# Optimization experiments

Measured on AMD Instinct MI355X. Metric: run time of the kernel, lower is better.

The kernel has to match this reference:

```python
import jax, jax.numpy as jnp
from jax import lax
import numpy as np

BOHR = 0.52917721067  # Angstrom per Bohr (au.BOHR)
DAMP_MUTUAL = 0.39
DAMP_FIELD = 0.7
N_ITER = 7  # fixed-point iterations for induced dipoles


def setup_inputs() -> dict:
    key = jax.random.key(0)
    N = 100000
    deg = 32
    E = N * deg
    k1, k2, k3, k4, k5, k6, k7 = jax.random.split(key, 7)
    edge_src = jax.random.randint(k1, (E,), 0, N)
    edge_dst = jax.random.randint(k2, (E,), 0, N)
    # realistic interatomic distances in [1, 6] Angstrom (avoid r ~ 0)
    distances = 1.0 + 5.0 * jax.random.uniform(k3, (E,), dtype=jnp.float32)
    u = jax.random.normal(k4, (E, 3), dtype=jnp.float32)
    u = u / jnp.linalg.norm(u, axis=-1, keepdims=True)
    vec = u * distances[:, None]  # consistent |vec| == distances
    polarisability = 0.5 + 1.5 * jax.random.uniform(k5, (N,), dtype=jnp.float32)
    charges = 0.3 * jax.random.normal(k6, (N,), dtype=jnp.float32)
    species = jax.random.randint(k7, (N,), 1, 10)
    return {
        "species": species,
        "edge_src": edge_src,
        "edge_dst": edge_dst,
        "distances": distances,
        "vec": vec,
        "polarisability": polarisability,
        "charges": charges,
    }


def reference(species, edge_src, edge_dst, distances, vec, polarisability, charges):
    N = polarisability.shape[0]
    # convert to atomic units
    rij = distances / BOHR                      # [E]
    vec_ij = vec / BOHR                         # [E,3]
    pol = polarisability.reshape(-1) / BOHR**3  # [N]

    # Thole damping: u_ij^3 = r^3 / sqrt(alpha_i * alpha_j)
    alpha_ij = pol[edge_src] * pol[edge_dst]
    uij3 = rij**3 / jnp.sqrt(alpha_ij)
    exp_m = jnp.exp(-DAMP_MUTUAL * uij3)
    l3_m = 1.0 - exp_m
    l5_m = 1.0 - (1.0 + DAMP_MUTUAL * uij3) * exp_m
    l3_f = 1.0 - jnp.exp(-DAMP_FIELD * uij3)

    inv_r3 = 1.0 / rij**3
    inv_r5 = inv_r3 / rij**2

    # permanent (charge) electric field at src atoms, Thole-damped
    e_edges = (l3_f * charges[edge_dst] * inv_r3)[:, None] * vec_ij  # [E,3]
    E0 = jax.ops.segment_sum(e_edges, edge_src, num_segments=N)      # [N,3]

    alpha = pol[:, None]  # isotropic polarisability [N,1]

    def matvec(mu):
        # Thole-damped dipole-dipole interaction tensor applied to mu: (T mu)_i
        mu_d = mu[edge_dst]                                   # [E,3]
        dot = jnp.sum(vec_ij * mu_d, axis=-1)                 # [E]
        t = (l3_m * inv_r3)[:, None] * mu_d \
            - (3.0 * l5_m * inv_r5 * dot)[:, None] * vec_ij   # [E,3]
        return jax.ops.segment_sum(t, edge_src, num_segments=N)

    # iterative induced dipoles: mu = alpha * (E0 - T mu)
    mu0 = alpha * E0

    def step(mu, _):
        return alpha * (E0 - matvec(mu)), None

    mu, _ = lax.scan(step, mu0, None, length=N_ITER)

    # per-atom polarisation energy: -1/2 mu . E0
    energy = -0.5 * jnp.sum(mu * E0, axis=-1)  # [N]
    return energy
```

## Files before the change

### kernel.cpp

```cpp
#include <hip/hip_runtime.h>
#include <hip/hip_fp16.h>


static constexpr float INV_B  = 1.0f / 0.52917721067f;
static constexpr float INV_B3 = INV_B * INV_B * INV_B;
static constexpr float DM = 0.39f;
static constexpr float DF = 0.7f;
static constexpr int   NITER = 7;
#define SCAN_B 1024
#define STAGE 2048
#define BUILD_T 512
#define MAXBUCK 512

__device__ inline unsigned packh2(float a, float b) {
    return (unsigned)__half_as_ushort(__float2half_rn(a)) |
           ((unsigned)__half_as_ushort(__float2half_rn(b)) << 16);
}
__device__ inline float unph_lo(unsigned u) {
    return __half2float(__ushort_as_half((unsigned short)(u & 0xFFFFu)));
}
__device__ inline float unph_hi(unsigned u) {
    return __half2float(__ushort_as_half((unsigned short)(u >> 16)));
}


__global__ void bhist_kernel(const int* __restrict__ esrc, int* __restrict__ hraw,
                             int* __restrict__ hpad, int E, int nbuck, int nblk, int chunk)
{
    __shared__ int cnt[MAXBUCK];
    int tid = threadIdx.x, blk = blockIdx.x;
    for (int b = tid; b < nbuck; b += blockDim.x) cnt[b] = 0;
    __syncthreads();
    int lo = blk * chunk, hi = min(E, lo + chunk);
    for (int i = lo + tid; i < hi; i += blockDim.x)
        atomicAdd(&cnt[esrc[i] >> 8], 1);
    __syncthreads();
    for (int b = tid; b < nbuck; b += blockDim.x) {
        int c = cnt[b];
        hraw[b * nblk + blk] = c;
        hpad[b * nblk + blk] = (c + 7) & ~7;
    }
}


__global__ void scan1_kernel(const int* __restrict__ in, int* __restrict__ excl,
                             int* __restrict__ blocksum, int n)
{
    __shared__ int sh[SCAN_B];
    int tid = threadIdx.x;
    int i = blockIdx.x * SCAN_B + tid;
    int v = (i < n) ? in[i] : 0;
    sh[tid] = v;
    __syncthreads();
    for (int off = 1; off < SCAN_B; off <<= 1) {
        int t = (tid >= off) ? sh[tid - off] : 0;
        __syncthreads();
        sh[tid] += t;
        __syncthreads();
    }
    if (i < n) excl[i] = sh[tid] - v;
    if (tid == SCAN_B - 1) blocksum[blockIdx.x] = sh[tid];
}

__global__ void scan2_kernel(int* __restrict__ blocksum, int nb)
{
    __shared__ int sh[1024];
    int tid = threadIdx.x;
    int v = (tid < nb) ? blocksum[tid] : 0;
    sh[tid] = v;
    __syncthreads();
    for (int off = 1; off < 1024; off <<= 1) {
        int t = (tid >= off) ? sh[tid - off] : 0;
        __syncthreads();
        sh[tid] += t;
        __syncthreads();
    }
    if (tid < nb) blocksum[tid] = sh[tid] - v;
}

__global__ void scan3_kernel(int* __restrict__ excl, const int* __restrict__ blocksum, int n)
{
    int i = blockIdx.x * SCAN_B + threadIdx.x;
    if (i < n) excl[i] += blocksum[blockIdx.x];
}

__global__ void bktptr_kernel(const int* __restrict__ hoffpad, const int* __restrict__ hpad,
                              int* __restrict__ bktptr, int* __restrict__ rowptr,
                              int nbuck, int nblk, int nScan, int N, int E)
{
    int b = blockIdx.x * blockDim.x + threadIdx.x;
    if (b < nbuck) bktptr[b] = hoffpad[b * nblk];
    if (b == nbuck) {
        bktptr[b] = hoffpad[nScan - 1] + hpad[nScan - 1];
        if (rowptr) rowptr[N] = E;
    }
}


__global__ __launch_bounds__(BUILD_T)
void build_kernel(const int* __restrict__ esrc, const int* __restrict__ edst,
                  const float* __restrict__ dist, const float* __restrict__ vec,
                  const float* __restrict__ pol, const float* __restrict__ chg,
                  const int* __restrict__ hoffpad, const int* __restrict__ hpad,
                  uint4* __restrict__ recs, int E, int nbuck, int nblk, int chunk)
{
    __shared__ uint4 stg[STAGE];
    __shared__ unsigned short sbuck[STAGE];
    __shared__ int wcur[MAXBUCK];
    __shared__ int shist[MAXBUCK];
    __shared__ int sbase[MAXBUCK];
    __shared__ int scur[MAXBUCK];
    __shared__ int wsum[8];
    int tid = threadIdx.x, blk = blockIdx.x;
    int lane = tid & 63, wav = tid >> 6;
    int lo = blk * chunk, hi = min(E, lo + chunk), cnt = hi - lo;

    if (tid < nbuck) wcur[tid] = hoffpad[tid * nblk + blk];
    __syncthreads();

    int nsb = (cnt + STAGE - 1) / STAGE;
    for (int sb = 0; sb < nsb; ++sb) {
        int s0 = sb * STAGE, s1 = min(cnt, s0 + STAGE), scnt = s1 - s0;
        if (tid < nbuck) shist[tid] = 0;
        __syncthreads();
        for (int i = s0 + tid; i < s1; i += BUILD_T)
            atomicAdd(&shist[esrc[lo + i] >> 8], 1);
        __syncthreads();
        int v = (tid < nbuck) ? shist[tid] : 0;
        int x = v;
        #pragma unroll
        for (int off = 1; off < 64; off <<= 1) {
            int t = __shfl_up(x, off);
            if (lane >= off) x += t;
        }
        if (lane == 63) wsum[wav] = x;
        __syncthreads();
        if (tid < 8) {
            int w = wsum[tid];
            #pragma unroll
            for (int off = 1; off < 8; off <<= 1) {
                int t = __shfl_up(w, off, 8);
                if (tid >= off) w += t;
            }
            wsum[tid] = w;
        }
        __syncthreads();
        int base = (wav > 0) ? wsum[wav - 1] : 0;
        if (tid < nbuck) {
            int ex = x + base - v;
            sbase[tid] = ex;
            scur[tid]  = ex;
        }
        __syncthreads();
        for (int i = s0 + tid; i < s1; i += BUILD_T) {
            int gi = lo + i;
            int s = esrc[gi], d = edst[gi];
            int b = s >> 8;
            float r  = dist[gi] * INV_B;
            float vx = vec[3*gi+0] * INV_B;
            float vy = vec[3*gi+1] * INV_B;
            float vz = vec[3*gi+2] * INV_B;
            float ps = pol[s] * INV_B3;
            float pd = pol[d] * INV_B3;
            float r2 = r * r;
            float r3 = r2 * r;
            float u  = r3 * rsqrtf(ps * pd);
            float em = __expf(-DM * u);
            float l3m = 1.0f - em;
            float l5m = 1.0f - (1.0f + DM * u) * em;
            float inv_r3 = 1.0f / r3;
            float inv_r5 = inv_r3 / r2;
            float c1 = l3m * inv_r3;
            float sw = sqrtf(3.0f * l5m * inv_r5);
            float ec = (1.0f - __expf(-DF * u)) * chg[d] * inv_r3;
            float g  = ec / sw;
            uint4 rc;
            rc.x = (unsigned)(d | ((s & 255) << 20));
            rc.y = __float_as_uint(c1);
            rc.z = packh2(sw * vx, sw * vy);
            rc.w = packh2(sw * vz, g);
            int sl = atomicAdd(&scur[b], 1);
            stg[sl]   = rc;
            sbuck[sl] = (unsigned short)b;
        }
        __syncthreads();
        for (int k = tid; k < scnt; k += BUILD_T) {
            int b = sbuck[k];
            recs[wcur[b] + (k - sbase[b])] = stg[k];
        }
        __syncthreads();
        if (tid < nbuck) wcur[tid] += shist[tid];
        __syncthreads();
    }
    if (tid < nbuck) {
        int base = hoffpad[tid * nblk + blk];
        int end  = base + hpad[tid * nblk + blk];
        for (int s2 = wcur[tid]; s2 < end; ++s2) recs[s2] = make_uint4(0, 0, 0, 0);
    }
}


__global__ void sort_kernel(const int* __restrict__ bktptr, const int* __restrict__ hoffraw,
                            int nblk, const uint4* __restrict__ recs_raw,
                            unsigned* __restrict__ srt,
                            int* __restrict__ rowptr, const float* __restrict__ pol,
                            float4* __restrict__ E0, float4* __restrict__ mu, int N)
{
    __shared__ int hist[256];
    __shared__ int scn[256];
    __shared__ int cur[256];
    __shared__ float acc[256 * 3];
    int tid = threadIdx.x, b = blockIdx.x;
    int j0 = bktptr[b], j1 = bktptr[b + 1];
    int tight0 = hoffraw[b * nblk];
    if (tid < 256) hist[tid] = 0;
    for (int k = tid; k < 768; k += blockDim.x) acc[k] = 0.f;
    __syncthreads();
    for (int j = j0 + tid; j < j1; j += blockDim.x) {
        uint4 rc = recs_raw[j];
        if (rc.y) atomicAdd(&hist[rc.x >> 20], 1);
    }
    __syncthreads();
    if (tid < 256) scn[tid] = hist[tid];
    __syncthreads();
    for (int off = 1; off < 256; off <<= 1) {
        int t = 0;
        if (tid < 256 && tid >= off) t = scn[tid - off];
        __syncthreads();
        if (tid < 256) scn[tid] += t;
        __syncthreads();
    }
    if (tid < 256) {
        int c = hist[tid];
        int beg = tight0 + scn[tid] - c;
        cur[tid] = beg;
        int row = b * 256 + tid;
        if (row < N) rowptr[row] = beg;
    }
    __syncthreads();
    for (int j = j0 + tid; j < j1; j += blockDim.x) {
        uint4 rc = recs_raw[j];
        if (rc.y) {
            int lr = (int)(rc.x >> 20);
            int slot = atomicAdd(&cur[lr], 1);
            float c1 = __uint_as_float(rc.y);
            float wx = unph_lo(rc.z), wy = unph_hi(rc.z);
            float wz = unph_lo(rc.w), g  = unph_hi(rc.w);
            srt[3*slot+0] = rc.x;
            srt[3*slot+1] = packh2(c1, wx);
            srt[3*slot+2] = packh2(wy, wz);
            atomicAdd(&acc[lr*3+0], g * wx);
            atomicAdd(&acc[lr*3+1], g * wy);
            atomicAdd(&acc[lr*3+2], g * wz);
        }
    }
    __syncthreads();
    if (tid < 256) {
        int row = b * 256 + tid;
        if (row < N) {
            float ax = acc[tid*3], ay = acc[tid*3+1], az = acc[tid*3+2];
            E0[row] = make_float4(ax, ay, az, 0.f);
            float a = pol[row] * INV_B3;
            mu[row] = make_float4(a * ax, a * ay, a * az, 0.f);
        }
    }
}


__global__ void mvg_kernel(const int* __restrict__ rowptr,
                           const unsigned* __restrict__ srt, const float4* __restrict__ E0,
                           const float* __restrict__ pol,
                           const float4* __restrict__ mu_in, float4* __restrict__ mu_out,
                           float* __restrict__ energy, int N, int final_iter)
{
    int tid  = threadIdx.x;
    int lane = tid & 15;
    int row  = (blockIdx.x * blockDim.x + tid) >> 4;
    if (row >= N) return;
    int r0 = rowptr[row], r1 = rowptr[row + 1];
    float ax = 0.f, ay = 0.f, az = 0.f;
    for (int j = r0 + lane; j < r1; j += 16) {
        unsigned pk = srt[3*j+0];
        unsigned w0 = srt[3*j+1];
        unsigned w1 = srt[3*j+2];
        float4 m = mu_in[pk & 0xFFFFF];
        float c1 = unph_lo(w0);
        float wx = unph_hi(w0), wy = unph_lo(w1), wz = unph_hi(w1);
        float dot = wx * m.x + wy * m.y + wz * m.z;
        ax += c1 * m.x - dot * wx;
        ay += c1 * m.y - dot * wy;
        az += c1 * m.z - dot * wz;
    }
    for (int msk = 8; msk >= 1; msk >>= 1) {
        ax += __shfl_xor(ax, msk);
        ay += __shfl_xor(ay, msk);
        az += __shfl_xor(az, msk);
    }
    if (lane == 0) {
        float4 e0 = E0[row];
        float a = pol[row] * INV_B3;
        float mx = a * (e0.x - ax);
        float my = a * (e0.y - ay);
        float mz = a * (e0.z - az);
        mu_out[row] = make_float4(mx, my, mz, 0.f);
        if (final_iter)
            energy[row] = -0.5f * (mx * e0.x + my * e0.y + mz * e0.z);
    }
}


__global__ void e0b_kernel(const int* __restrict__ bktptr, const uint4* __restrict__ recs,
                           const float* __restrict__ pol,
                           float4* __restrict__ E0, float4* __restrict__ mu, int N)
{
    __shared__ float acc[256 * 3];
    int tid = threadIdx.x, b = blockIdx.x;
    for (int k = tid; k < 768; k += 256) acc[k] = 0.f;
    __syncthreads();
    int j0 = bktptr[b], j1 = bktptr[b + 1];
    for (int j = j0 + tid; j < j1; j += 256) {
        uint4 rc = recs[j];
        int lr = (int)(rc.x >> 20) & 255;
        float g = unph_hi(rc.w);
        atomicAdd(&acc[lr*3+0], g * unph_lo(rc.z));
        atomicAdd(&acc[lr*3+1], g * unph_hi(rc.z));
        atomicAdd(&acc[lr*3+2], g * unph_lo(rc.w));
    }
    __syncthreads();
    int r = b * 256 + tid;
    if (r < N) {
        float ax = acc[tid*3], ay = acc[tid*3+1], az = acc[tid*3+2];
        E0[r] = make_float4(ax, ay, az, 0.f);
        float a = pol[r] * INV_B3;
        mu[r] = make_float4(a * ax, a * ay, a * az, 0.f);
    }
}

__global__ void mvb_kernel(const int* __restrict__ bktptr, const uint4* __restrict__ recs,
                           const float4* __restrict__ E0, const float* __restrict__ pol,
                           const float4* __restrict__ mu_in, float4* __restrict__ mu_out,
                           float* __restrict__ energy, int N, int final_iter)
{
    __shared__ float acc[256 * 3];
    int tid = threadIdx.x, b = blockIdx.x;
    for (int k = tid; k < 768; k += 256) acc[k] = 0.f;
    __syncthreads();
    int j0 = bktptr[b], j1 = bktptr[b + 1];
    for (int j = j0 + tid; j < j1; j += 256) {
        uint4 rc = recs[j];
        float4 m = mu_in[rc.x & 0xFFFFF];
        float c1 = __uint_as_float(rc.y);
        float wx = unph_lo(rc.z), wy = unph_hi(rc.z), wz = unph_lo(rc.w);
        float dot = wx * m.x + wy * m.y + wz * m.z;
        int lr = (int)(rc.x >> 20) & 255;
        atomicAdd(&acc[lr*3+0], c1 * m.x - dot * wx);
        atomicAdd(&acc[lr*3+1], c1 * m.y - dot * wy);
        atomicAdd(&acc[lr*3+2], c1 * m.z - dot * wz);
    }
    __syncthreads();
    int r = b * 256 + tid;
    if (r < N) {
        float4 e0 = E0[r];
        float a = pol[r] * INV_B3;
        float mx = a * (e0.x - acc[tid*3+0]);
        float my = a * (e0.y - acc[tid*3+1]);
        float mz = a * (e0.z - acc[tid*3+2]);
        mu_out[r] = make_float4(mx, my, mz, 0.f);
        if (final_iter)
            energy[r] = -0.5f * (mx * e0.x + my * e0.y + mz * e0.z);
    }
}


__global__ void fb_e0_kernel(const int* esrc, const int* edst, const float* dist,
                             const float* vec, const float* pol, const float* chg,
                             float4* E0, int E)
{
    int e = blockIdx.x * blockDim.x + threadIdx.x;
    if (e >= E) return;
    int s = esrc[e], d = edst[e];
    float r  = dist[e] * INV_B;
    float vx = vec[3*e+0]*INV_B, vy = vec[3*e+1]*INV_B, vz = vec[3*e+2]*INV_B;
    float r3 = r*r*r;
    float u  = r3 * rsqrtf(pol[s]*INV_B3 * pol[d]*INV_B3);
    float ec = (1.0f - __expf(-DF*u)) * chg[d] / r3;
    atomicAdd(&E0[s].x, ec*vx); atomicAdd(&E0[s].y, ec*vy); atomicAdd(&E0[s].z, ec*vz);
}

__global__ void fb_init_kernel(const float* pol, const float4* E0, float4* mu, float4* acc, int N)
{
    int i = blockIdx.x * blockDim.x + threadIdx.x;
    if (i >= N) return;
    float a = pol[i]*INV_B3; float4 e0 = E0[i];
    mu[i]  = make_float4(a*e0.x, a*e0.y, a*e0.z, 0.f);
    acc[i] = make_float4(0.f,0.f,0.f,0.f);
}

__global__ void fb_matvec_kernel(const int* esrc, const int* edst, const float* dist,
                                 const float* vec, const float* pol,
                                 const float4* mu, float4* acc, int E)
{
    int e = blockIdx.x * blockDim.x + threadIdx.x;
    if (e >= E) return;
    int s = esrc[e], d = edst[e];
    float r  = dist[e]*INV_B;
    float vx = vec[3*e+0]*INV_B, vy = vec[3*e+1]*INV_B, vz = vec[3*e+2]*INV_B;
    float r2 = r*r, r3 = r2*r;
    float u  = r3 * rsqrtf(pol[s]*INV_B3 * pol[d]*INV_B3);
    float em = __expf(-DM*u);
    float c1 = (1.0f - em) / r3;
    float c2 = 3.0f * (1.0f - (1.0f + DM*u)*em) / (r3*r2);
    float4 m = mu[d];
    float k = c2 * (vx*m.x + vy*m.y + vz*m.z);
    atomicAdd(&acc[s].x, c1*m.x - k*vx);
    atomicAdd(&acc[s].y, c1*m.y - k*vy);
    atomicAdd(&acc[s].z, c1*m.z - k*vz);
}

__global__ void fb_update_kernel(const float* pol, const float4* E0, float4* acc,
                                 float4* mu, float* energy, int N, int final_iter)
{
    int i = blockIdx.x * blockDim.x + threadIdx.x;
    if (i >= N) return;
    float a = pol[i]*INV_B3; float4 e0 = E0[i]; float4 ac = acc[i];
    float mx = a*(e0.x-ac.x), my = a*(e0.y-ac.y), mz = a*(e0.z-ac.z);
    mu[i]  = make_float4(mx,my,mz,0.f);
    acc[i] = make_float4(0.f,0.f,0.f,0.f);
    if (final_iter) energy[i] = -0.5f*(mx*e0.x + my*e0.y + mz*e0.z);
}


static inline size_t align_up(size_t x, size_t a) { return (x + a - 1) & ~(a - 1); }

struct Layout {
    int chunk, nblk, nScan, g1;
    size_t o_hpad, o_hoffpad, o_bsum1, o_bkt, o_E0, o_mua, o_mub, o_hraw, o_recsraw;
    size_t need_mid;
    size_t o_hoffraw, o_bsum2, o_rowptr, o_srt;
    size_t need_sort;
};

static Layout make_layout(int E, int N, int nbuck, int chunk)
{
    Layout L;
    L.chunk = chunk;
    L.nblk  = (E + chunk - 1) / chunk;
    L.nScan = nbuck * L.nblk;
    L.g1    = (L.nScan + SCAN_B - 1) / SCAN_B;
    size_t Epad = (size_t)E + 7u * (size_t)L.nScan;
    size_t off = 0;
    auto carve = [&](size_t bytes) { size_t o = off; off = align_up(off + bytes, 256); return o; };
    L.o_hpad    = carve((size_t)L.nScan * 4);
    L.o_hoffpad = carve((size_t)L.nScan * 4);
    L.o_bsum1   = carve(1024 * 4);
    L.o_bkt     = carve((size_t)(nbuck + 1) * 4);
    L.o_E0      = carve((size_t)N * 16);
    L.o_mua     = carve((size_t)N * 16);
    L.o_mub     = carve((size_t)N * 16);
    L.o_hraw    = carve((size_t)L.nScan * 4);
    L.o_recsraw = carve(Epad * 16);
    L.need_mid  = off;
    L.o_hoffraw = carve((size_t)L.nScan * 4);
    L.o_bsum2   = carve(1024 * 4);
    L.o_rowptr  = carve((size_t)(N + 1) * 4);
    L.o_srt     = carve((size_t)E * 12);
    L.need_sort = off;
    return L;
}

extern "C" void kernel_launch(void* const* d_in, const int* in_sizes, int n_in,
                              void* d_out, int out_size, void* d_ws, size_t ws_size,
                              hipStream_t stream)
{
    const int*   esrc = (const int*)  d_in[1];
    const int*   edst = (const int*)  d_in[2];
    const float* dist = (const float*)d_in[3];
    const float* vec  = (const float*)d_in[4];
    const float* pol  = (const float*)d_in[5];
    const float* chg  = (const float*)d_in[6];
    const int E = in_sizes[1];
    const int N = in_sizes[5];
    float* out = (float*)d_out;

    const int nbuck = (N + 255) >> 8;

    const int cand[3] = {8192, 16384, 32768};
    Layout L{}; bool ok_sort = false, ok_mid = false;
    for (int ci = 0; ci < 3; ++ci) {
        Layout t = make_layout(E, N, nbuck, cand[ci]);
        bool shp = (nbuck <= MAXBUCK) && (t.g1 <= 1024) && (nbuck >= 1) && (N < (1 << 20));
        if (shp && ws_size >= t.need_sort) { L = t; ok_sort = true; break; }
    }
    if (!ok_sort) {
        Layout t = make_layout(E, N, nbuck, 32768);
        bool shp = (nbuck <= MAXBUCK) && (t.g1 <= 1024) && (nbuck >= 1) && (N < (1 << 20));
        if (shp && ws_size >= t.need_mid) { L = t; ok_mid = true; }
    }

    char* ws = (char*)d_ws;

    if (ok_sort || ok_mid) {
        int*    hpad    = (int*)   (ws + L.o_hpad);
        int*    hoffpad = (int*)   (ws + L.o_hoffpad);
        int*    bsum1   = (int*)   (ws + L.o_bsum1);
        int*    bktptr  = (int*)   (ws + L.o_bkt);
        float4* E0      = (float4*)(ws + L.o_E0);
        float4* mu_a    = (float4*)(ws + L.o_mua);
        float4* mu_b    = (float4*)(ws + L.o_mub);
        int*    hraw    = (int*)   (ws + L.o_hraw);
        uint4*  recsraw = (uint4*) (ws + L.o_recsraw);
        int*    rowptr  = ok_sort ? (int*)(ws + L.o_rowptr) : nullptr;

        bhist_kernel<<<L.nblk, BUILD_T, 0, stream>>>(esrc, hraw, hpad, E, nbuck,
                                                     L.nblk, L.chunk);
        scan1_kernel<<<L.g1, SCAN_B, 0, stream>>>(hpad, hoffpad, bsum1, L.nScan);
        scan2_kernel<<<1, 1024, 0, stream>>>(bsum1, L.g1);
        scan3_kernel<<<L.g1, SCAN_B, 0, stream>>>(hoffpad, bsum1, L.nScan);
        bktptr_kernel<<<(nbuck + 256) / 256, 256, 0, stream>>>(hoffpad, hpad, bktptr,
                                                               rowptr, nbuck, L.nblk,
                                                               L.nScan, N, E);
        build_kernel<<<L.nblk, BUILD_T, 0, stream>>>(esrc, edst, dist, vec, pol, chg,
                                                     hoffpad, hpad, recsraw,
                                                     E, nbuck, L.nblk, L.chunk);

        if (ok_sort) {
            int*      hoffraw = (int*)     (ws + L.o_hoffraw);
            int*      bsum2   = (int*)     (ws + L.o_bsum2);
            unsigned* srt     = (unsigned*)(ws + L.o_srt);

            scan1_kernel<<<L.g1, SCAN_B, 0, stream>>>(hraw, hoffraw, bsum2, L.nScan);
            scan2_kernel<<<1, 1024, 0, stream>>>(bsum2, L.g1);
            scan3_kernel<<<L.g1, SCAN_B, 0, stream>>>(hoffraw, bsum2, L.nScan);
            sort_kernel<<<nbuck, 512, 0, stream>>>(bktptr, hoffraw, L.nblk, recsraw,
                                                   srt, rowptr, pol, E0, mu_a, N);

            const int NG16 = (N + 15) / 16;
            float4* min_ = mu_a; float4* mout_ = mu_b;
            for (int it = 0; it < NITER; ++it) {
                mvg_kernel<<<NG16, 256, 0, stream>>>(rowptr, srt, E0, pol,
                                                     min_, mout_, out, N, it == NITER - 1);
                float4* t = min_; min_ = mout_; mout_ = t;
            }
        } else {
            e0b_kernel<<<nbuck, 256, 0, stream>>>(bktptr, recsraw, pol, E0, mu_a, N);
            float4* min_ = mu_a; float4* mout_ = mu_b;
            for (int it = 0; it < NITER; ++it) {
                mvb_kernel<<<nbuck, 256, 0, stream>>>(bktptr, recsraw, E0, pol,
                                                      min_, mout_, out, N, it == NITER - 1);
                float4* t = min_; min_ = mout_; mout_ = t;
            }
        }
    } else {
        float4* E0  = (float4*)(ws);
        float4* mu  = (float4*)(ws + (size_t)N * 16);
        float4* acc = (float4*)(ws + (size_t)N * 32);
        const int EB = 256, NB = 256;
        const int EG = (E + EB - 1) / EB;
        const int NG = (N + NB - 1) / NB;
        hipMemsetAsync(E0, 0, (size_t)N * 16, stream);
        fb_e0_kernel<<<EG, EB, 0, stream>>>(esrc, edst, dist, vec, pol, chg, E0, E);
        fb_init_kernel<<<NG, NB, 0, stream>>>(pol, E0, mu, acc, N);
        for (int it = 0; it < NITER; ++it) {
            fb_matvec_kernel<<<EG, EB, 0, stream>>>(esrc, edst, dist, vec, pol, mu, acc, E);
            fb_update_kernel<<<NG, NB, 0, stream>>>(pol, E0, acc, mu, out, N, it == NITER - 1);
        }
    }
}
```

Before: 333.1 us.

## Drop padded bucket layout and second scan pass in edge binning

Removes the 8-aligned padding of per-block bucket segments, so the build phase needs only one histogram and one scan instead of separate padded and raw scans. The sort kernel no longer filters zero padding records or reads a second offset table, and it replaces its shared-memory Hillis-Steele scan with a wave-shuffle scan. This cuts three kernel launches, the padding zero-fill, and the extra record traffic. The staging buffer is also doubled, which raises LDS use per build block and may lower occupancy. The mvb fallback path loses its alignment padding, which it may have relied on.

```diff
diff --git a/kernel.cpp b/kernel.cpp
--- a/kernel.cpp
+++ b/kernel.cpp
@@ -8,7 +8,7 @@
 static constexpr float DF = 0.7f;
 static constexpr int   NITER = 7;
 #define SCAN_B 1024
-#define STAGE 2048
+#define STAGE 4096
 #define BUILD_T 512
 #define MAXBUCK 512
 
@@ -24,8 +24,8 @@
 }
 
 
-__global__ void bhist_kernel(const int* __restrict__ esrc, int* __restrict__ hraw,
-                             int* __restrict__ hpad, int E, int nbuck, int nblk, int chunk)
+__global__ void bhist_kernel(const int* __restrict__ esrc, int* __restrict__ h,
+                             int E, int nbuck, int nblk, int chunk)
 {
     __shared__ int cnt[MAXBUCK];
     int tid = threadIdx.x, blk = blockIdx.x;
@@ -35,11 +35,8 @@
     for (int i = lo + tid; i < hi; i += blockDim.x)
         atomicAdd(&cnt[esrc[i] >> 8], 1);
     __syncthreads();
-    for (int b = tid; b < nbuck; b += blockDim.x) {
-        int c = cnt[b];
-        hraw[b * nblk + blk] = c;
-        hpad[b * nblk + blk] = (c + 7) & ~7;
-    }
+    for (int b = tid; b < nbuck; b += blockDim.x)
+        h[b * nblk + blk] = cnt[b];
 }
 
 
@@ -84,14 +81,15 @@
     if (i < n) excl[i] += blocksum[blockIdx.x];
 }
 
-__global__ void bktptr_kernel(const int* __restrict__ hoffpad, const int* __restrict__ hpad,
+
+__global__ void bktptr_kernel(const int* __restrict__ hoff,
                               int* __restrict__ bktptr, int* __restrict__ rowptr,
-                              int nbuck, int nblk, int nScan, int N, int E)
+                              int nbuck, int nblk, int N, int E)
 {
     int b = blockIdx.x * blockDim.x + threadIdx.x;
-    if (b < nbuck) bktptr[b] = hoffpad[b * nblk];
+    if (b < nbuck) bktptr[b] = hoff[b * nblk];
     if (b == nbuck) {
-        bktptr[b] = hoffpad[nScan - 1] + hpad[nScan - 1];
+        bktptr[b] = E;
         if (rowptr) rowptr[N] = E;
     }
 }
@@ -101,7 +99,7 @@
 void build_kernel(const int* __restrict__ esrc, const int* __restrict__ edst,
                   const float* __restrict__ dist, const float* __restrict__ vec,
                   const float* __restrict__ pol, const float* __restrict__ chg,
-                  const int* __restrict__ hoffpad, const int* __restrict__ hpad,
+                  const int* __restrict__ hoff,
                   uint4* __restrict__ recs, int E, int nbuck, int nblk, int chunk)
 {
     __shared__ uint4 stg[STAGE];
@@ -115,7 +113,7 @@
     int lane = tid & 63, wav = tid >> 6;
     int lo = blk * chunk, hi = min(E, lo + chunk), cnt = hi - lo;
 
-    if (tid < nbuck) wcur[tid] = hoffpad[tid * nblk + blk];
+    if (tid < nbuck) wcur[tid] = hoff[tid * nblk + blk];
     __syncthreads();
 
     int nsb = (cnt + STAGE - 1) / STAGE;
@@ -192,47 +190,50 @@
         if (tid < nbuck) wcur[tid] += shist[tid];
         __syncthreads();
     }
-    if (tid < nbuck) {
-        int base = hoffpad[tid * nblk + blk];
-        int end  = base + hpad[tid * nblk + blk];
-        for (int s2 = wcur[tid]; s2 < end; ++s2) recs[s2] = make_uint4(0, 0, 0, 0);
-    }
-}
-
-
-__global__ void sort_kernel(const int* __restrict__ bktptr, const int* __restrict__ hoffraw,
-                            int nblk, const uint4* __restrict__ recs_raw,
+}
+
+
+__global__ void sort_kernel(const int* __restrict__ bktptr,
+                            const uint4* __restrict__ recs_raw,
                             unsigned* __restrict__ srt,
                             int* __restrict__ rowptr, const float* __restrict__ pol,
                             float4* __restrict__ E0, float4* __restrict__ mu, int N)
 {
     __shared__ int hist[256];
-    __shared__ int scn[256];
     __shared__ int cur[256];
     __shared__ float acc[256 * 3];
+    __shared__ int wsum4[4];
     int tid = threadIdx.x, b = blockIdx.x;
+    int lane = tid & 63, wav = tid >> 6;
     int j0 = bktptr[b], j1 = bktptr[b + 1];
-    int tight0 = hoffraw[b * nblk];
     if (tid < 256) hist[tid] = 0;
     for (int k = tid; k < 768; k += blockDim.x) acc[k] = 0.f;
     __syncthreads();
-    for (int j = j0 + tid; j < j1; j += blockDim.x) {
-        uint4 rc = recs_raw[j];
-        if (rc.y) atomicAdd(&hist[rc.x >> 20], 1);
-    }
-    __syncthreads();
-    if (tid < 256) scn[tid] = hist[tid];
-    __syncthreads();
-    for (int off = 1; off < 256; off <<= 1) {
-        int t = 0;
-        if (tid < 256 && tid >= off) t = scn[tid - off];
-        __syncthreads();
-        if (tid < 256) scn[tid] += t;
-        __syncthreads();
-    }
+    for (int j = j0 + tid; j < j1; j += blockDim.x)
+        atomicAdd(&hist[recs_raw[j].x >> 20], 1);
+    __syncthreads();
+    int v = (tid < 256) ? hist[tid] : 0;
+    int x = v;
+    #pragma unroll
+    for (int off = 1; off < 64; off <<= 1) {
+        int t = __shfl_up(x, off);
+        if (lane >= off) x += t;
+    }
+    if (lane == 63 && wav < 4) wsum4[wav] = x;
+    __syncthreads();
+    if (tid < 4) {
+        int w = wsum4[tid];
+        #pragma unroll
+        for (int off = 1; off < 4; off <<= 1) {
+            int t = __shfl_up(w, off, 4);
+            if (tid >= off) w += t;
+        }
+        wsum4[tid] = w;
+    }
+    __syncthreads();
     if (tid < 256) {
-        int c = hist[tid];
-        int beg = tight0 + scn[tid] - c;
+        int base = (wav > 0) ? wsum4[wav - 1] : 0;
+        int beg = j0 + x + base - v;
         cur[tid] = beg;
         int row = b * 256 + tid;
         if (row < N) rowptr[row] = beg;
@@ -240,19 +241,17 @@
     __syncthreads();
     for (int j = j0 + tid; j < j1; j += blockDim.x) {
         uint4 rc = recs_raw[j];
-        if (rc.y) {
-            int lr = (int)(rc.x >> 20);
-            int slot = atomicAdd(&cur[lr], 1);
-            float c1 = __uint_as_float(rc.y);
-            float wx = unph_lo(rc.z), wy = unph_hi(rc.z);
-            float wz = unph_lo(rc.w), g  = unph_hi(rc.w);
-            srt[3*slot+0] = rc.x;
-            srt[3*slot+1] = packh2(c1, wx);
-            srt[3*slot+2] = packh2(wy, wz);
-            atomicAdd(&acc[lr*3+0], g * wx);
-            atomicAdd(&acc[lr*3+1], g * wy);
-            atomicAdd(&acc[lr*3+2], g * wz);
-        }
+        int lr = (int)(rc.x >> 20);
+        int slot = atomicAdd(&cur[lr], 1);
+        float c1 = __uint_as_float(rc.y);
+        float wx = unph_lo(rc.z), wy = unph_hi(rc.z);
+        float wz = unph_lo(rc.w), g  = unph_hi(rc.w);
+        srt[3*slot+0] = rc.x;
+        srt[3*slot+1] = packh2(c1, wx);
+        srt[3*slot+2] = packh2(wy, wz);
+        atomicAdd(&acc[lr*3+0], g * wx);
+        atomicAdd(&acc[lr*3+1], g * wy);
+        atomicAdd(&acc[lr*3+2], g * wz);
     }
     __syncthreads();
     if (tid < 256) {
@@ -434,9 +433,9 @@
 
 struct Layout {
     int chunk, nblk, nScan, g1;
-    size_t o_hpad, o_hoffpad, o_bsum1, o_bkt, o_E0, o_mua, o_mub, o_hraw, o_recsraw;
+    size_t o_h, o_hoff, o_bsum, o_bkt, o_E0, o_mua, o_mub, o_recs;
     size_t need_mid;
-    size_t o_hoffraw, o_bsum2, o_rowptr, o_srt;
+    size_t o_rowptr, o_srt;
     size_t need_sort;
 };
 
@@ -447,23 +446,19 @@
     L.nblk  = (E + chunk - 1) / chunk;
     L.nScan = nbuck * L.nblk;
     L.g1    = (L.nScan + SCAN_B - 1) / SCAN_B;
-    size_t Epad = (size_t)E + 7u * (size_t)L.nScan;
     size_t off = 0;
     auto carve = [&](size_t bytes) { size_t o = off; off = align_up(off + bytes, 256); return o; };
-    L.o_hpad    = carve((size_t)L.nScan * 4);
-    L.o_hoffpad = carve((size_t)L.nScan * 4);
-    L.o_bsum1   = carve(1024 * 4);
-    L.o_bkt     = carve((size_t)(nbuck + 1) * 4);
-    L.o_E0      = carve((size_t)N * 16);
-    L.o_mua     = carve((size_t)N * 16);
-    L.o_mub     = carve((size_t)N * 16);
-    L.o_hraw    = carve((size_t)L.nScan * 4);
-    L.o_recsraw = carve(Epad * 16);
-    L.need_mid  = off;
-    L.o_hoffraw = carve((size_t)L.nScan * 4);
-    L.o_bsum2   = carve(1024 * 4);
-    L.o_rowptr  = carve((size_t)(N + 1) * 4);
-    L.o_srt     = carve((size_t)E * 12);
+    L.o_h      = carve((size_t)L.nScan * 4);
+    L.o_hoff   = carve((size_t)L.nScan * 4);
+    L.o_bsum   = carve(1024 * 4);
+    L.o_bkt    = carve((size_t)(nbuck + 1) * 4);
+    L.o_E0     = carve((size_t)N * 16);
+    L.o_mua    = carve((size_t)N * 16);
+    L.o_mub    = carve((size_t)N * 16);
+    L.o_recs   = carve((size_t)E * 16);
+    L.need_mid = off;
+    L.o_rowptr = carve((size_t)(N + 1) * 4);
+    L.o_srt    = carve((size_t)E * 12);
     L.need_sort = off;
     return L;
 }
@@ -500,39 +495,30 @@
     char* ws = (char*)d_ws;
 
     if (ok_sort || ok_mid) {
-        int*    hpad    = (int*)   (ws + L.o_hpad);
-        int*    hoffpad = (int*)   (ws + L.o_hoffpad);
-        int*    bsum1   = (int*)   (ws + L.o_bsum1);
-        int*    bktptr  = (int*)   (ws + L.o_bkt);
-        float4* E0      = (float4*)(ws + L.o_E0);
-        float4* mu_a    = (float4*)(ws + L.o_mua);
-        float4* mu_b    = (float4*)(ws + L.o_mub);
-        int*    hraw    = (int*)   (ws + L.o_hraw);
-        uint4*  recsraw = (uint4*) (ws + L.o_recsraw);
-        int*    rowptr  = ok_sort ? (int*)(ws + L.o_rowptr) : nullptr;
-
-        bhist_kernel<<<L.nblk, BUILD_T, 0, stream>>>(esrc, hraw, hpad, E, nbuck,
-                                                     L.nblk, L.chunk);
-        scan1_kernel<<<L.g1, SCAN_B, 0, stream>>>(hpad, hoffpad, bsum1, L.nScan);
-        scan2_kernel<<<1, 1024, 0, stream>>>(bsum1, L.g1);
-        scan3_kernel<<<L.g1, SCAN_B, 0, stream>>>(hoffpad, bsum1, L.nScan);
-        bktptr_kernel<<<(nbuck + 256) / 256, 256, 0, stream>>>(hoffpad, hpad, bktptr,
-                                                               rowptr, nbuck, L.nblk,
-                                                               L.nScan, N, E);
+        int*    h      = (int*)   (ws + L.o_h);
+        int*    hoff   = (int*)   (ws + L.o_hoff);
+        int*    bsum   = (int*)   (ws + L.o_bsum);
+        int*    bktptr = (int*)   (ws + L.o_bkt);
+        float4* E0     = (float4*)(ws + L.o_E0);
+        float4* mu_a   = (float4*)(ws + L.o_mua);
+        float4* mu_b   = (float4*)(ws + L.o_mub);
+        uint4*  recs   = (uint4*) (ws + L.o_recs);
+        int*    rowptr = ok_sort ? (int*)(ws + L.o_rowptr) : nullptr;
+
+        bhist_kernel<<<L.nblk, BUILD_T, 0, stream>>>(esrc, h, E, nbuck, L.nblk, L.chunk);
+        scan1_kernel<<<L.g1, SCAN_B, 0, stream>>>(h, hoff, bsum, L.nScan);
+        scan2_kernel<<<1, 1024, 0, stream>>>(bsum, L.g1);
+        scan3_kernel<<<L.g1, SCAN_B, 0, stream>>>(hoff, bsum, L.nScan);
+        bktptr_kernel<<<(nbuck + 256) / 256, 256, 0, stream>>>(hoff, bktptr, rowptr,
+                                                               nbuck, L.nblk, N, E);
         build_kernel<<<L.nblk, BUILD_T, 0, stream>>>(esrc, edst, dist, vec, pol, chg,
-                                                     hoffpad, hpad, recsraw,
-                                                     E, nbuck, L.nblk, L.chunk);
+                                                     hoff, recs, E, nbuck, L.nblk, L.chunk);
 
         if (ok_sort) {
-            int*      hoffraw = (int*)     (ws + L.o_hoffraw);
-            int*      bsum2   = (int*)     (ws + L.o_bsum2);
-            unsigned* srt     = (unsigned*)(ws + L.o_srt);
-
-            scan1_kernel<<<L.g1, SCAN_B, 0, stream>>>(hraw, hoffraw, bsum2, L.nScan);
-            scan2_kernel<<<1, 1024, 0, stream>>>(bsum2, L.g1);
-            scan3_kernel<<<L.g1, SCAN_B, 0, stream>>>(hoffraw, bsum2, L.nScan);
-            sort_kernel<<<nbuck, 512, 0, stream>>>(bktptr, hoffraw, L.nblk, recsraw,
-                                                   srt, rowptr, pol, E0, mu_a, N);
+            unsigned* srt = (unsigned*)(ws + L.o_srt);
+
+            sort_kernel<<<nbuck, 512, 0, stream>>>(bktptr, recs, srt, rowptr,
+                                                   pol, E0, mu_a, N);
 
             const int NG16 = (N + 15) / 16;
             float4* min_ = mu_a; float4* mout_ = mu_b;
@@ -542,10 +528,10 @@
                 float4* t = min_; min_ = mout_; mout_ = t;
             }
         } else {
-            e0b_kernel<<<nbuck, 256, 0, stream>>>(bktptr, recsraw, pol, E0, mu_a, N);
+            e0b_kernel<<<nbuck, 256, 0, stream>>>(bktptr, recs, pol, E0, mu_a, N);
             float4* min_ = mu_a; float4* mout_ = mu_b;
             for (int it = 0; it < NITER; ++it) {
-                mvb_kernel<<<nbuck, 256, 0, stream>>>(bktptr, recsraw, E0, pol,
+                mvb_kernel<<<nbuck, 256, 0, stream>>>(bktptr, recs, E0, pol,
                                                       min_, mout_, out, N, it == NITER - 1);
                 float4* t = min_; min_ = mout_; mout_ = t;
             }
```

New measurement: 324.3 us. -2.7%, faster.
